# Kernel tuning notes

Measured on AMD Instinct MI355X. Metric: run time of the kernel, lower is better.

## Reference

```python
import jax, jax.numpy as jnp
import numpy as np

N = 50000      # nodes
DEG = 16       # fixed out-degree per row
E = N * DEG    # edges (CSR nnz)
H = 128        # hidden_size
NH = 8         # num_heads


def setup_inputs() -> dict:
    key = jax.random.key(0)
    ks = jax.random.split(key, 8)
    s = 1.0 / np.sqrt(H)
    h = jax.random.normal(ks[0], (N, H), jnp.float32)
    Wq = jax.random.normal(ks[1], (H, H), jnp.float32) * s
    bq = jax.random.normal(ks[2], (H,), jnp.float32) * 0.02
    Wk = jax.random.normal(ks[3], (H, H), jnp.float32) * s
    bk = jax.random.normal(ks[4], (H,), jnp.float32) * 0.02
    Wv = jax.random.normal(ks[5], (H, H), jnp.float32) * s
    bv = jax.random.normal(ks[6], (H,), jnp.float32) * 0.02
    row_ptr = jnp.arange(N + 1, dtype=jnp.int32) * DEG            # fixed-degree CSR
    col_ind = jax.random.randint(ks[7], (E,), 0, N, dtype=jnp.int32)
    return {"h": h, "Wq": Wq, "bq": bq, "Wk": Wk, "bk": bk, "Wv": Wv, "bv": bv,
            "row_ptr": row_ptr, "col_ind": col_ind, "num_heads": NH}


def reference(h, Wq, bq, Wk, bk, Wv, bv, row_ptr, col_ind, num_heads):
    n = h.shape[0]
    hidden = h.shape[1]
    head_dim = hidden // num_heads
    scaling = head_dim ** (-0.5)
    e = col_ind.shape[0]
    # CSR nnz -> row index per edge
    row = (jnp.searchsorted(row_ptr, jnp.arange(e, dtype=row_ptr.dtype), side="right") - 1).astype(jnp.int32)

    # projections; reshape to (N, head_dim, num_heads) exactly as in the torch code
    q = ((h @ Wq.T + bq) * scaling).reshape(n, head_dim, num_heads)
    k = (h @ Wk.T + bk).reshape(n, head_dim, num_heads)
    v = (h @ Wv.T + bv).reshape(n, head_dim, num_heads)

    # bsddmm: per-edge, per-head dot product over head_dim
    scores = jnp.einsum("edh,edh->eh", q[row], k[col_ind])      # [E, NH]

    # sparse row-wise softmax (segment softmax over edges of each row)
    m = jax.ops.segment_max(scores, row, num_segments=n)        # [N, NH]
    ex = jnp.exp(scores - m[row])
    denom = jax.ops.segment_sum(ex, row, num_segments=n)        # [N, NH]
    attn = ex / denom[row]                                      # [E, NH]

    # bspmm: out[i] = sum_{j in nbr(i)} attn[ij] * v[j]
    out = jax.ops.segment_sum(attn[:, None, :] * v[col_ind], row, num_segments=n)  # [N, head_dim, NH]
    return out.reshape(n, -1)
```

## Files before the change

kernel.cpp:

```cpp
#include <hip/hip_runtime.h>
#include <hip/hip_bf16.h>


typedef unsigned short ushort_t;
typedef unsigned int uint32;
typedef short short8 __attribute__((ext_vector_type(8)));
typedef short short4v __attribute__((ext_vector_type(4)));
typedef float f32x4 __attribute__((ext_vector_type(4)));

#define HID 128
#define DEG 16
#define OSTRIDE_LDS 132

__device__ __forceinline__ float bf2f(ushort_t u) {
  uint32 x = ((uint32)u) << 16;
  return __builtin_bit_cast(float, x);
}
__device__ __forceinline__ ushort_t f2bf(float f) {
  uint32 u = __builtin_bit_cast(uint32, f);
  u += 0x7fffu + ((u >> 16) & 1u);
  return (ushort_t)(u >> 16);
}

__device__ __forceinline__ void split2(float x, float y, uint32& hi, uint32& lo) {
  __hip_bfloat162 h2 = __float22bfloat162_rn(float2{x, y});
  __builtin_memcpy(&hi, &h2, 4);
  float hx = __builtin_bit_cast(float, hi << 16);
  float hy = __builtin_bit_cast(float, hi & 0xffff0000u);
  __hip_bfloat162 l2 = __float22bfloat162_rn(float2{x - hx, y - hy});
  __builtin_memcpy(&lo, &l2, 4);
}

__device__ __forceinline__ void split8v(float4 a, float4 b, short8& hi, short8& lo) {
  uint32* hu = (uint32*)&hi;
  uint32* lu = (uint32*)&lo;
  split2(a.x, a.y, hu[0], lu[0]);
  split2(a.z, a.w, hu[1], lu[1]);
  split2(b.x, b.y, hu[2], lu[2]);
  split2(b.z, b.w, hu[3], lu[3]);
}

__device__ __forceinline__ void split8p(const float* __restrict__ p, short8& hi, short8& lo) {
  float4 a = *(const float4*)p;
  float4 b = *(const float4*)(p + 4);
  split8v(a, b, hi, lo);
}

__global__ __launch_bounds__(256) void prep_kernel(
    const float* __restrict__ Wq, const float* __restrict__ Wk,
    const float* __restrict__ Wv,
    ushort_t* __restrict__ whi, ushort_t* __restrict__ wlo) {
  const int idx8 = (blockIdx.x * 256 + threadIdx.x) * 8;
  const float* W = (idx8 < 16384) ? Wq : (idx8 < 32768) ? Wk : Wv;
  const int off = idx8 & 16383;
  short8 hi, lo;
  split8p(W + off, hi, lo);
  *(short8*)(whi + idx8) = hi;
  *(short8*)(wlo + idx8) = lo;
}

__global__ __launch_bounds__(256) void qkv_kernel(
    const float* __restrict__ h,
    const float* __restrict__ bq, const float* __restrict__ bk,
    const float* __restrict__ bv,
    const ushort_t* __restrict__ whi, const ushort_t* __restrict__ wlo,
    ushort_t* __restrict__ qs, ushort_t* __restrict__ ks, ushort_t* __restrict__ vs,
    int n) {
  __shared__ __align__(16) float4 lds_f4[4][1024];

  const int which = blockIdx.y;
  const float* __restrict__ bias = (which == 0) ? bq : (which == 1) ? bk : bv;
  ushort_t* __restrict__ outp = (which == 0) ? qs : (which == 1) ? ks : vs;
  const int ostride = (which == 0) ? 256 : 128;
  const float scale = (which == 0) ? 0.25f : 1.0f;
  const ushort_t* __restrict__ Wh = whi + which * 16384;
  const ushort_t* __restrict__ Wl = wlo + which * 16384;

  const int wave = threadIdx.x >> 6;
  const int l = threadIdx.x & 63;
  const int lm = l & 15;
  const int lq = l >> 4;
  const int m0 = blockIdx.x * 128 + wave * 32;

  {
    const int r = l & 31;
    const int chalf = l >> 5;
    int grow = m0 + r; if (grow >= n) grow = n - 1;
    const float* gbase = h + (size_t)grow * HID;
    char* lbase = (char*)&lds_f4[wave][0];
#pragma unroll
    for (int j = 0; j < 16; j++) {
      const int c = j * 2 + chalf;
      const float* gp = gbase + c * 4;
      __builtin_amdgcn_global_load_lds(
          (const __attribute__((address_space(1))) void*)gp,
          (__attribute__((address_space(3))) void*)(lbase + j * 1024 + l * 16),
          16, 0, 0);
    }
  }
  asm volatile("s_waitcnt vmcnt(0)" ::: "memory");
  __builtin_amdgcn_wave_barrier();

  const float4* lw = &lds_f4[wave][0];

  f32x4 acc[2][8];
#pragma unroll
  for (int f = 0; f < 2; f++)
#pragma unroll
    for (int t = 0; t < 8; t++) acc[f][t] = (f32x4){0.f, 0.f, 0.f, 0.f};

#pragma unroll
  for (int kt = 0; kt < 4; kt++) {
    const int c0 = kt * 8 + lq * 2;
    float4 x0 = lw[(c0 + 0) * 32 + lm];
    float4 y0 = lw[(c0 + 1) * 32 + lm];
    float4 x1 = lw[(c0 + 0) * 32 + 16 + lm];
    float4 y1 = lw[(c0 + 1) * 32 + 16 + lm];
    short8 ah0, al0, ah1, al1;
    split8v(x0, y0, ah0, al0);
    split8v(x1, y1, ah1, al1);
    const int boff = kt * 32 + lq * 8 + lm * HID;
#pragma unroll
    for (int t = 0; t < 8; t++) {
      short8 bh = *(const short8*)(Wh + t * 16 * HID + boff);
      short8 bl = *(const short8*)(Wl + t * 16 * HID + boff);
      acc[0][t] = __builtin_amdgcn_mfma_f32_16x16x32_bf16(ah0, bh, acc[0][t], 0, 0, 0);
      acc[0][t] = __builtin_amdgcn_mfma_f32_16x16x32_bf16(ah0, bl, acc[0][t], 0, 0, 0);
      acc[0][t] = __builtin_amdgcn_mfma_f32_16x16x32_bf16(al0, bh, acc[0][t], 0, 0, 0);
      acc[1][t] = __builtin_amdgcn_mfma_f32_16x16x32_bf16(ah1, bh, acc[1][t], 0, 0, 0);
      acc[1][t] = __builtin_amdgcn_mfma_f32_16x16x32_bf16(ah1, bl, acc[1][t], 0, 0, 0);
      acc[1][t] = __builtin_amdgcn_mfma_f32_16x16x32_bf16(al1, bh, acc[1][t], 0, 0, 0);
    }
  }

  ushort_t* lo_ = (ushort_t*)lw;
#pragma unroll
  for (int t = 0; t < 8; t++) {
    const int col = t * 16 + lm;
    const float bv_ = bias[col];
#pragma unroll
    for (int f = 0; f < 2; f++) {
#pragma unroll
      for (int r = 0; r < 4; r++) {
        lo_[(f * 16 + lq * 4 + r) * OSTRIDE_LDS + col] = f2bf((acc[f][t][r] + bv_) * scale);
      }
    }
  }
  asm volatile("s_waitcnt lgkmcnt(0)" ::: "memory");
  __builtin_amdgcn_wave_barrier();

  const int rr = l >> 5;
  const int ch = l & 31;
#pragma unroll
  for (int it = 0; it < 16; it++) {
    const int rw = it * 2 + rr;
    const int grow = m0 + rw;
    short4v val = *(short4v*)(lo_ + rw * OSTRIDE_LDS + ch * 4);
    if (grow < n) *(short4v*)(outp + (size_t)grow * ostride + ch * 4) = val;
  }
}

__global__ __launch_bounds__(256) void attn_kernel(
    const int* __restrict__ col_ind,
    const ushort_t* __restrict__ qs, const ushort_t* __restrict__ ks,
    const ushort_t* __restrict__ vs, float* __restrict__ out, int n) {
  __shared__ __align__(16) float lds_attn[4 * DEG * 8];

  const int wv = threadIdx.x >> 6;
  const int l = threadIdx.x & 63;
  const int lm = l & 15;
  const int lq = l >> 4;

  int row = blockIdx.x * 4 + wv;
  if (row >= n) row = n - 1;
  const int eb = row * DEG;

  const int cm = col_ind[eb + lm];
  const ushort_t* kp = ks + (size_t)cm * HID + lq * 8;
  const ushort_t* qp = qs + (size_t)row * 256;

  short8 af[4];
  ushort_t qv[4];
#pragma unroll
  for (int kt = 0; kt < 4; kt++) {
    af[kt] = *(const short8*)(kp + kt * 32);
    qv[kt] = (lm < 8) ? qp[kt * 32 + lq * 8 + lm] : (ushort_t)0;
  }

  uint32 vreg[DEG];
#pragma unroll
  for (int e = 0; e < DEG; e++) {
    const int c = col_ind[eb + e];
    vreg[e] = *(const uint32*)(vs + (size_t)c * HID + 2 * l);
  }

  f32x4 acc = (f32x4){0.f, 0.f, 0.f, 0.f};
#pragma unroll
  for (int kt = 0; kt < 4; kt++) {
    short8 bf;
#pragma unroll
    for (int j = 0; j < 8; j++) bf[j] = (lm == j) ? (short)qv[kt] : (short)0;
    acc = __builtin_amdgcn_mfma_f32_16x16x32_bf16(af[kt], bf, acc, 0, 0, 0);
  }

  float m = fmaxf(fmaxf(acc[0], acc[1]), fmaxf(acc[2], acc[3]));
  m = fmaxf(m, __shfl_xor(m, 16, 64));
  m = fmaxf(m, __shfl_xor(m, 32, 64));
  float e0 = __expf(acc[0] - m), e1 = __expf(acc[1] - m);
  float e2 = __expf(acc[2] - m), e3 = __expf(acc[3] - m);
  float s = e0 + e1 + e2 + e3;
  s += __shfl_xor(s, 16, 64);
  s += __shfl_xor(s, 32, 64);
  const float inv = 1.0f / s;

  float* ap = &lds_attn[wv * (DEG * 8)];
  if (lm < 8) {
    ap[(lq * 4 + 0) * 8 + lm] = e0 * inv;
    ap[(lq * 4 + 1) * 8 + lm] = e1 * inv;
    ap[(lq * 4 + 2) * 8 + lm] = e2 * inv;
    ap[(lq * 4 + 3) * 8 + lm] = e3 * inv;
  }
  asm volatile("s_waitcnt lgkmcnt(0)" ::: "memory");
  __builtin_amdgcn_wave_barrier();

  const int h0 = 2 * (l & 3);
  float o0 = 0.f, o1 = 0.f;
#pragma unroll
  for (int e = 0; e < DEG; e++) {
    const float2 at = *(const float2*)(ap + e * 8 + h0);
    o0 += at.x * bf2f((ushort_t)(vreg[e] & 0xffffu));
    o1 += at.y * bf2f((ushort_t)(vreg[e] >> 16));
  }

  float2 o = {o0, o1};
  *(float2*)(out + (size_t)row * HID + 2 * l) = o;
}

extern "C" void kernel_launch(void* const* d_in, const int* in_sizes, int n_in,
                              void* d_out, int out_size, void* d_ws, size_t ws_size,
                              hipStream_t stream) {
  const float* h  = (const float*)d_in[0];
  const float* Wq = (const float*)d_in[1];
  const float* bq = (const float*)d_in[2];
  const float* Wk = (const float*)d_in[3];
  const float* bk = (const float*)d_in[4];
  const float* Wv = (const float*)d_in[5];
  const float* bv = (const float*)d_in[6];
  const int* col_ind = (const int*)d_in[8];

  const int n = in_sizes[0] / HID;

  ushort_t* ks  = (ushort_t*)d_ws;
  ushort_t* vs  = ks + (size_t)n * HID;
  ushort_t* whi = vs + (size_t)n * HID;
  ushort_t* wlo = whi + 3 * 16384;
  ushort_t* qs  = (ushort_t*)d_out;
  float* outf   = (float*)d_out;

  prep_kernel<<<24, 256, 0, stream>>>(Wq, Wk, Wv, whi, wlo);
  dim3 g1((n + 127) / 128, 3);
  qkv_kernel<<<g1, 256, 0, stream>>>(h, bq, bk, bv, whi, wlo, qs, ks, vs, n);
  attn_kernel<<<(n + 3) / 4, 256, 0, stream>>>(col_ind, qs, ks, vs, outf, n);
}
```

Baseline: 199.4 us.

## Fuse Q/K/V projections into one kernel with LDS-staged shared weights

Replaces the three-way grid split over Q/K/V with a single kernel per 128-row tile. It loads and splits h into bf16 hi/lo fragments once in registers, then loops over the three projections. Weight hi and lo tiles are staged cooperatively into LDS through global_load_lds and shared by all four waves, so each wave no longer reads weights from global memory. h is read from global once instead of three times, at the cost of block-wide syncs between the stages and a larger LDS footprint that could lower occupancy.

Result: faster. 172.2 us (-13.7%).

```diff
diff --git a/kernel.cpp b/kernel.cpp
--- a/kernel.cpp
+++ b/kernel.cpp
@@ -59,22 +59,15 @@
   *(short8*)(wlo + idx8) = lo;
 }
 
-__global__ __launch_bounds__(256) void qkv_kernel(
+__global__ __launch_bounds__(256) void qkv_fused_kernel(
     const float* __restrict__ h,
     const float* __restrict__ bq, const float* __restrict__ bk,
     const float* __restrict__ bv,
     const ushort_t* __restrict__ whi, const ushort_t* __restrict__ wlo,
     ushort_t* __restrict__ qs, ushort_t* __restrict__ ks, ushort_t* __restrict__ vs,
     int n) {
-  __shared__ __align__(16) float4 lds_f4[4][1024];
-
-  const int which = blockIdx.y;
-  const float* __restrict__ bias = (which == 0) ? bq : (which == 1) ? bk : bv;
-  ushort_t* __restrict__ outp = (which == 0) ? qs : (which == 1) ? ks : vs;
-  const int ostride = (which == 0) ? 256 : 128;
-  const float scale = (which == 0) ? 0.25f : 1.0f;
-  const ushort_t* __restrict__ Wh = whi + which * 16384;
-  const ushort_t* __restrict__ Wl = wlo + which * 16384;
+  __shared__ __align__(16) char lds_b[32 * 1024];
+  __shared__ ushort_t lds_r[4][32 * OSTRIDE_LDS];
 
   const int wave = threadIdx.x >> 6;
   const int l = threadIdx.x & 63;
@@ -82,81 +75,101 @@
   const int lq = l >> 4;
   const int m0 = blockIdx.x * 128 + wave * 32;
 
-  {
-    const int r = l & 31;
-    const int chalf = l >> 5;
-    int grow = m0 + r; if (grow >= n) grow = n - 1;
-    const float* gbase = h + (size_t)grow * HID;
-    char* lbase = (char*)&lds_f4[wave][0];
-#pragma unroll
-    for (int j = 0; j < 16; j++) {
-      const int c = j * 2 + chalf;
-      const float* gp = gbase + c * 4;
+  int ar0 = m0 + lm;        if (ar0 >= n) ar0 = n - 1;
+  int ar1 = m0 + 16 + lm;   if (ar1 >= n) ar1 = n - 1;
+  const float* ap0 = h + (size_t)ar0 * HID + lq * 8;
+  const float* ap1 = h + (size_t)ar1 * HID + lq * 8;
+  short8 ah0[4], al0[4], ah1[4], al1[4];
+#pragma unroll
+  for (int kt = 0; kt < 4; kt++) {
+    split8p(ap0 + kt * 32, ah0[kt], al0[kt]);
+    split8p(ap1 + kt * 32, ah1[kt], al1[kt]);
+  }
+
+#pragma unroll 1
+  for (int p = 0; p < 3; p++) {
+    const ushort_t* __restrict__ Wh = whi + p * 16384;
+    const ushort_t* __restrict__ Wl = wlo + p * 16384;
+    const float* __restrict__ bias = (p == 0) ? bq : (p == 1) ? bk : bv;
+    ushort_t* __restrict__ outp = (p == 0) ? qs : (p == 1) ? ks : vs;
+    const int ostride = (p == 0) ? 256 : 128;
+    const float scale = (p == 0) ? 0.25f : 1.0f;
+
+    f32x4 acc[2][8];
+#pragma unroll
+    for (int f = 0; f < 2; f++)
+#pragma unroll
+      for (int t = 0; t < 8; t++) acc[f][t] = (f32x4){0.f, 0.f, 0.f, 0.f};
+
+#pragma unroll
+    for (int jj = 0; jj < 8; jj++) {
+      const int j = wave * 8 + jj, t = j >> 2, kt = j & 3;
+      const ushort_t* gp = Wh + (t * 16 + lm) * HID + kt * 32 + lq * 8;
       __builtin_amdgcn_global_load_lds(
           (const __attribute__((address_space(1))) void*)gp,
-          (__attribute__((address_space(3))) void*)(lbase + j * 1024 + l * 16),
+          (__attribute__((address_space(3))) void*)(lds_b + j * 1024 + l * 16),
           16, 0, 0);
     }
-  }
-  asm volatile("s_waitcnt vmcnt(0)" ::: "memory");
-  __builtin_amdgcn_wave_barrier();
-
-  const float4* lw = &lds_f4[wave][0];
-
-  f32x4 acc[2][8];
-#pragma unroll
-  for (int f = 0; f < 2; f++)
-#pragma unroll
-    for (int t = 0; t < 8; t++) acc[f][t] = (f32x4){0.f, 0.f, 0.f, 0.f};
-
-#pragma unroll
-  for (int kt = 0; kt < 4; kt++) {
-    const int c0 = kt * 8 + lq * 2;
-    float4 x0 = lw[(c0 + 0) * 32 + lm];
-    float4 y0 = lw[(c0 + 1) * 32 + lm];
-    float4 x1 = lw[(c0 + 0) * 32 + 16 + lm];
-    float4 y1 = lw[(c0 + 1) * 32 + 16 + lm];
-    short8 ah0, al0, ah1, al1;
-    split8v(x0, y0, ah0, al0);
-    split8v(x1, y1, ah1, al1);
-    const int boff = kt * 32 + lq * 8 + lm * HID;
+    __syncthreads();
+#pragma unroll
+    for (int kt = 0; kt < 4; kt++) {
+#pragma unroll
+      for (int t = 0; t < 8; t++) {
+        short8 bh = *(const short8*)(lds_b + (t * 4 + kt) * 1024 + l * 16);
+        acc[0][t] = __builtin_amdgcn_mfma_f32_16x16x32_bf16(ah0[kt], bh, acc[0][t], 0, 0, 0);
+        acc[0][t] = __builtin_amdgcn_mfma_f32_16x16x32_bf16(al0[kt], bh, acc[0][t], 0, 0, 0);
+        acc[1][t] = __builtin_amdgcn_mfma_f32_16x16x32_bf16(ah1[kt], bh, acc[1][t], 0, 0, 0);
+        acc[1][t] = __builtin_amdgcn_mfma_f32_16x16x32_bf16(al1[kt], bh, acc[1][t], 0, 0, 0);
+      }
+    }
+    __syncthreads();
+
+#pragma unroll
+    for (int jj = 0; jj < 8; jj++) {
+      const int j = wave * 8 + jj, t = j >> 2, kt = j & 3;
+      const ushort_t* gp = Wl + (t * 16 + lm) * HID + kt * 32 + lq * 8;
+      __builtin_amdgcn_global_load_lds(
+          (const __attribute__((address_space(1))) void*)gp,
+          (__attribute__((address_space(3))) void*)(lds_b + j * 1024 + l * 16),
+          16, 0, 0);
+    }
+    __syncthreads();
+#pragma unroll
+    for (int kt = 0; kt < 4; kt++) {
+#pragma unroll
+      for (int t = 0; t < 8; t++) {
+        short8 bl = *(const short8*)(lds_b + (t * 4 + kt) * 1024 + l * 16);
+        acc[0][t] = __builtin_amdgcn_mfma_f32_16x16x32_bf16(ah0[kt], bl, acc[0][t], 0, 0, 0);
+        acc[1][t] = __builtin_amdgcn_mfma_f32_16x16x32_bf16(ah1[kt], bl, acc[1][t], 0, 0, 0);
+      }
+    }
+    __syncthreads();
+
+    ushort_t* lo_ = lds_r[wave];
 #pragma unroll
     for (int t = 0; t < 8; t++) {
-      short8 bh = *(const short8*)(Wh + t * 16 * HID + boff);
-      short8 bl = *(const short8*)(Wl + t * 16 * HID + boff);
-      acc[0][t] = __builtin_amdgcn_mfma_f32_16x16x32_bf16(ah0, bh, acc[0][t], 0, 0, 0);
-      acc[0][t] = __builtin_amdgcn_mfma_f32_16x16x32_bf16(ah0, bl, acc[0][t], 0, 0, 0);
-      acc[0][t] = __builtin_amdgcn_mfma_f32_16x16x32_bf16(al0, bh, acc[0][t], 0, 0, 0);
-      acc[1][t] = __builtin_amdgcn_mfma_f32_16x16x32_bf16(ah1, bh, acc[1][t], 0, 0, 0);
-      acc[1][t] = __builtin_amdgcn_mfma_f32_16x16x32_bf16(ah1, bl, acc[1][t], 0, 0, 0);
-      acc[1][t] = __builtin_amdgcn_mfma_f32_16x16x32_bf16(al1, bh, acc[1][t], 0, 0, 0);
-    }
-  }
-
-  ushort_t* lo_ = (ushort_t*)lw;
-#pragma unroll
-  for (int t = 0; t < 8; t++) {
-    const int col = t * 16 + lm;
-    const float bv_ = bias[col];
-#pragma unroll
-    for (int f = 0; f < 2; f++) {
-#pragma unroll
-      for (int r = 0; r < 4; r++) {
-        lo_[(f * 16 + lq * 4 + r) * OSTRIDE_LDS + col] = f2bf((acc[f][t][r] + bv_) * scale);
+      const int col = t * 16 + lm;
+      const float bv_ = bias[col];
+#pragma unroll
+      for (int f = 0; f < 2; f++) {
+#pragma unroll
+        for (int r = 0; r < 4; r++) {
+          lo_[(f * 16 + lq * 4 + r) * OSTRIDE_LDS + col] = f2bf((acc[f][t][r] + bv_) * scale);
+        }
       }
     }
-  }
-  asm volatile("s_waitcnt lgkmcnt(0)" ::: "memory");
-  __builtin_amdgcn_wave_barrier();
-
-  const int rr = l >> 5;
-  const int ch = l & 31;
-#pragma unroll
-  for (int it = 0; it < 16; it++) {
-    const int rw = it * 2 + rr;
-    const int grow = m0 + rw;
-    short4v val = *(short4v*)(lo_ + rw * OSTRIDE_LDS + ch * 4);
-    if (grow < n) *(short4v*)(outp + (size_t)grow * ostride + ch * 4) = val;
+    asm volatile("s_waitcnt lgkmcnt(0)" ::: "memory");
+    __builtin_amdgcn_wave_barrier();
+
+    const int rr = l >> 5;
+    const int ch = l & 31;
+#pragma unroll
+    for (int it = 0; it < 16; it++) {
+      const int rw = it * 2 + rr;
+      const int grow = m0 + rw;
+      short4v val = *(short4v*)(lo_ + rw * OSTRIDE_LDS + ch * 4);
+      if (grow < n) *(short4v*)(outp + (size_t)grow * ostride + ch * 4) = val;
+    }
   }
 }
 
@@ -258,7 +271,6 @@
   float* outf   = (float*)d_out;
 
   prep_kernel<<<24, 256, 0, stream>>>(Wq, Wk, Wv, whi, wlo);
-  dim3 g1((n + 127) / 128, 3);
-  qkv_kernel<<<g1, 256, 0, stream>>>(h, bq, bk, bv, whi, wlo, qs, ks, vs, n);
+  qkv_fused_kernel<<<(n + 127) / 128, 256, 0, stream>>>(h, bq, bk, bv, whi, wlo, qs, ks, vs, n);
   attn_kernel<<<(n + 3) / 4, 256, 0, stream>>>(col_ind, qs, ks, vs, outf, n);
 }
```
